# Kernel optimization log

Measured on AMD Instinct MI355X. Metric: run time of the kernel, lower is better.

The kernel has to match this reference:

```python
import jax, jax.numpy as jnp
import numpy as np

N_NODES = 100000


def gcn_conv(x, edge_index, W, b, num_nodes):
    # PyG GCNConv: h = x @ W; add self-loops; symmetric deg^-1/2 normalization;
    # out[dst] = sum_{src->dst} norm * h[src] + b
    h = x @ W
    loop = jnp.arange(num_nodes)
    src = jnp.concatenate([edge_index[0], loop])
    dst = jnp.concatenate([edge_index[1], loop])
    deg = jax.ops.segment_sum(jnp.ones_like(dst, dtype=h.dtype), dst, num_segments=num_nodes)
    dinv = jnp.where(deg > 0, jax.lax.rsqrt(deg), 0.0)
    norm = dinv[src] * dinv[dst]  # [E+N]
    msg = h[src] * norm[:, None]  # gather + scale
    out = jax.ops.segment_sum(msg, dst, num_segments=num_nodes)
    return out + b


def setup_inputs() -> dict:
    key = jax.random.key(0)
    k1, k2, k3, k4 = jax.random.split(key, 4)
    E = 3200000
    F_IN, HID, CLS = 512, 16, 7
    x = jax.random.normal(k1, (N_NODES, F_IN), dtype=jnp.float32)
    edge_index = jax.random.randint(k2, (2, E), 0, N_NODES, dtype=jnp.int64)
    W1 = jax.random.normal(k3, (F_IN, HID), dtype=jnp.float32) / np.sqrt(F_IN)
    b1 = jnp.zeros((HID,), dtype=jnp.float32)
    W2 = jax.random.normal(k4, (HID, CLS), dtype=jnp.float32) / np.sqrt(HID)
    b2 = jnp.zeros((CLS,), dtype=jnp.float32)
    return {"x": x, "edge_index": edge_index, "W1": W1, "b1": b1, "W2": W2, "b2": b2}


def reference(x, edge_index, W1, b1, W2, b2):
    h = gcn_conv(x, edge_index, W1, b1, N_NODES)
    h = jax.nn.relu(h)
    # dropout is identity in eval mode (p=0.5, training=False)
    out = gcn_conv(h, edge_index, W2, b2, N_NODES)
    return out
```

## Files before the change

### kernel.cpp

```cpp
#include <hip/hip_runtime.h>

#define N_NODES 100000
#define F_IN 512
#define HID 16
#define CLS 7

#define BK_SHIFT 8
#define BK_NODES 256
#define NBK ((N_NODES + BK_NODES - 1) / BK_NODES)
#define BK_CAP 9216

#define ADD4(a, v) { (a).x += (v).x; (a).y += (v).y; (a).z += (v).z; (a).w += (v).w; }
#define FMA4(acc, sc, wv) { (acc).x += (sc)*(wv).x; (acc).y += (sc)*(wv).y; (acc).z += (sc)*(wv).z; (acc).w += (sc)*(wv).w; }

__global__ void detect_i64_kernel(const unsigned int* __restrict__ idx32,
                                  int* __restrict__ flag, int n_check,
                                  int* __restrict__ cursor) {
    for (int i = threadIdx.x; i < NBK; i += blockDim.x) cursor[i] = 0;
    __shared__ unsigned int s;
    if (threadIdx.x == 0) s = 0u;
    __syncthreads();
    unsigned int v = 0u;
    for (int i = threadIdx.x; i < n_check; i += blockDim.x)
        v |= idx32[2 * i + 1];
    atomicOr(&s, v);
    __syncthreads();
    if (threadIdx.x == 0) *flag = (s == 0u) ? 1 : 0;
}

#define SB_T 512
#define SB_TILE 8192
#define SB_EPT (SB_TILE / SB_T)

__global__ __launch_bounds__(SB_T) void scatter_bin_kernel(const void* __restrict__ eidx,
                                                           long long E,
                                                           const int* __restrict__ flag,
                                                           int* __restrict__ cursor,
                                                           unsigned int* __restrict__ binned) {
    __shared__ int hist[NBK];
    __shared__ int gcur[NBK];
    const int is64 = *flag;
    const int tid = threadIdx.x;
    const long long tileBeg = (long long)blockIdx.x * SB_TILE;
    const bool evE = ((E & 1LL) == 0LL);

    for (int i = tid; i < NBK; i += SB_T) hist[i] = 0;
    __syncthreads();

    unsigned int vv[SB_EPT];
    int bb[SB_EPT];

#pragma unroll
    for (int j = 0; j < SB_EPT / 2; j++) {
        long long e = tileBeg + (long long)j * (2 * SB_T) + 2 * tid;
        int s0 = 0, d0 = 0, s1 = 0, d1 = 0;
        const bool ok0 = e < E, ok1 = (e + 1) < E;
        if (is64) {
            const long long* p = (const long long*)eidx;
            if (ok1 && evE) {
                longlong2 sp = *(const longlong2*)(p + e);
                longlong2 dp = *(const longlong2*)(p + E + e);
                s0 = (int)sp.x; s1 = (int)sp.y; d0 = (int)dp.x; d1 = (int)dp.y;
            } else {
                if (ok0) { s0 = (int)p[e];     d0 = (int)p[E + e]; }
                if (ok1) { s1 = (int)p[e + 1]; d1 = (int)p[E + e + 1]; }
            }
        } else {
            const int* p = (const int*)eidx;
            if (ok1 && evE) {
                int2 sp = *(const int2*)(p + e);
                int2 dp = *(const int2*)(p + E + e);
                s0 = sp.x; s1 = sp.y; d0 = dp.x; d1 = dp.y;
            } else {
                if (ok0) { s0 = p[e];     d0 = p[E + e]; }
                if (ok1) { s1 = p[e + 1]; d1 = p[E + e + 1]; }
            }
        }
        if (ok0) {
            int b = d0 >> BK_SHIFT;
            bb[2 * j] = b;
            vv[2 * j] = ((unsigned int)(d0 & (BK_NODES - 1)) << 17) | (unsigned int)s0;
            atomicAdd(&hist[b], 1);
        } else bb[2 * j] = -1;
        if (ok1) {
            int b = d1 >> BK_SHIFT;
            bb[2 * j + 1] = b;
            vv[2 * j + 1] = ((unsigned int)(d1 & (BK_NODES - 1)) << 17) | (unsigned int)s1;
            atomicAdd(&hist[b], 1);
        } else bb[2 * j + 1] = -1;
    }
    __syncthreads();
    for (int i = tid; i < NBK; i += SB_T)
        gcur[i] = hist[i] ? (i * BK_CAP + atomicAdd(&cursor[i], hist[i])) : 0;
    __syncthreads();
#pragma unroll
    for (int j = 0; j < SB_EPT; j++) {
        int b = bb[j];
        if (b >= 0) {
            int pos = atomicAdd(&gcur[b], 1);
            if (pos < (b + 1) * BK_CAP)
                binned[pos] = vv[j];
        }
    }
}

__global__ __launch_bounds__(512) void csr_build_kernel(const int* __restrict__ cursor,
                                                        unsigned int* __restrict__ binned,
                                                        float* __restrict__ dinv,
                                                        int* __restrict__ rowptr,
                                                        int* __restrict__ degA) {
    __shared__ unsigned int stage[BK_CAP];
    __shared__ int hist[BK_NODES];
    __shared__ int scanv[BK_NODES];
    __shared__ int curs[BK_NODES];
    const int tid = threadIdx.x;
    const int b = blockIdx.x;
    const int base = b * BK_CAP;
    int cnt = cursor[b];
    if (cnt > BK_CAP) cnt = BK_CAP;
    if (tid < BK_NODES) hist[tid] = 0;
    __syncthreads();
    const int cnt4 = cnt >> 2;
    for (int i = tid; i < cnt4; i += 512) {
        uint4 u = ((const uint4*)(binned + base))[i];
        ((uint4*)stage)[i] = u;
        atomicAdd(&hist[u.x >> 17], 1);
        atomicAdd(&hist[u.y >> 17], 1);
        atomicAdd(&hist[u.z >> 17], 1);
        atomicAdd(&hist[u.w >> 17], 1);
    }
    for (int i = (cnt4 << 2) + tid; i < cnt; i += 512) {
        unsigned int u = binned[base + i];
        stage[i] = u;
        atomicAdd(&hist[u >> 17], 1);
    }
    __syncthreads();
    if (tid < BK_NODES) scanv[tid] = hist[tid];
    __syncthreads();
    for (int off = 1; off < BK_NODES; off <<= 1) {
        int a = 0;
        if (tid < BK_NODES && tid >= off) a = scanv[tid - off];
        __syncthreads();
        if (tid < BK_NODES) scanv[tid] += a;
        __syncthreads();
    }
    if (tid < BK_NODES) {
        int e = scanv[tid] - hist[tid];
        curs[tid] = e;
        int g = b * BK_NODES + tid;
        if (g < N_NODES) {
            rowptr[g] = base + e;
            degA[g] = hist[tid];
            dinv[g] = rsqrtf((float)(hist[tid] + 1));
        }
    }
    __syncthreads();
    for (int i = tid; i < cnt4; i += 512) {
        uint4 u = ((const uint4*)stage)[i];
        int p0 = atomicAdd(&curs[(int)(u.x >> 17)], 1); binned[base + p0] = u.x & 0x1FFFFu;
        int p1 = atomicAdd(&curs[(int)(u.y >> 17)], 1); binned[base + p1] = u.y & 0x1FFFFu;
        int p2 = atomicAdd(&curs[(int)(u.z >> 17)], 1); binned[base + p2] = u.z & 0x1FFFFu;
        int p3 = atomicAdd(&curs[(int)(u.w >> 17)], 1); binned[base + p3] = u.w & 0x1FFFFu;
    }
    for (int i = (cnt4 << 2) + tid; i < cnt; i += 512) {
        unsigned int u = stage[i];
        int p = atomicAdd(&curs[(int)(u >> 17)], 1);
        binned[base + p] = u & 0x1FFFFu;
    }
}

#define G1_ROWS 128
#define G1_KC 32
#define G1_LDX (G1_KC + 4)

__global__ __launch_bounds__(256) void gemm1_kernel(const float* __restrict__ x,
                                                    const float* __restrict__ W1,
                                                    const float* __restrict__ dinv,
                                                    float* __restrict__ h1s) {
    __shared__ float Ws[F_IN * HID];
    __shared__ float xs[G1_ROWS][G1_LDX];
    const int tid = threadIdx.x;
    const int rowBase = blockIdx.x * G1_ROWS;

#pragma unroll
    for (int it = 0; it < 8; it++) {
        int f = it * 256 + tid;
        ((float4*)Ws)[f] = ((const float4*)W1)[f];
    }

    const int r  = tid >> 2;
    const int j4 = tid & 3;
    float4 accA = make_float4(0.f, 0.f, 0.f, 0.f);
    float4 accB = make_float4(0.f, 0.f, 0.f, 0.f);
    const float4* Wf4 = (const float4*)Ws;

    for (int kc = 0; kc < F_IN; kc += G1_KC) {
        __syncthreads();
#pragma unroll
        for (int it = 0; it < 4; it++) {
            int f = it * 256 + tid;
            int row = f >> 3;
            int c4 = f & 7;
            int grow = rowBase + row;
            if (grow >= N_NODES) grow = N_NODES - 1;
            *((float4*)&xs[row][c4 * 4]) = ((const float4*)(x + (long long)grow * F_IN + kc))[c4];
        }
        __syncthreads();
#pragma unroll
        for (int k4 = 0; k4 < G1_KC / 4; k4++) {
            float4 xa = *(const float4*)&xs[r][k4 * 4];
            float4 xb = *(const float4*)&xs[r + 64][k4 * 4];
            int kb = (kc + k4 * 4) * 4 + j4;
            float4 w0 = Wf4[kb];
            float4 w1 = Wf4[kb + 4];
            float4 w2 = Wf4[kb + 8];
            float4 w3 = Wf4[kb + 12];
            FMA4(accA, xa.x, w0); FMA4(accA, xa.y, w1);
            FMA4(accA, xa.z, w2); FMA4(accA, xa.w, w3);
            FMA4(accB, xb.x, w0); FMA4(accB, xb.y, w1);
            FMA4(accB, xb.z, w2); FMA4(accB, xb.w, w3);
        }
    }
    int g0 = rowBase + r;
    if (g0 < N_NODES) {
        float dn = dinv[g0];
        ((float4*)(h1s + (long long)g0 * HID))[j4] =
            make_float4(accA.x * dn, accA.y * dn, accA.z * dn, accA.w * dn);
    }
    int g1 = rowBase + 64 + r;
    if (g1 < N_NODES) {
        float dn = dinv[g1];
        ((float4*)(h1s + (long long)g1 * HID))[j4] =
            make_float4(accB.x * dn, accB.y * dn, accB.z * dn, accB.w * dn);
    }
}

#define A1_NODES 64

__global__ __launch_bounds__(256) void agg1_gemm2_kernel(const int* __restrict__ rowptr,
                                                         const int* __restrict__ degA,
                                                         const int* __restrict__ csr_src,
                                                         const float* __restrict__ h1s,
                                                         const float* __restrict__ dinv,
                                                         const float* __restrict__ b1,
                                                         const float* __restrict__ W2,
                                                         float* __restrict__ h2s) {
    __shared__ float W2s[HID][8];
    __shared__ float t_lds[A1_NODES][HID + 1];
    const int tid = threadIdx.x;
    if (tid < HID * 8) {
        int j = tid >> 3, c = tid & 7;
        W2s[j][c] = (c < CLS) ? W2[j * CLS + c] : 0.f;
    }
    const int ln = tid >> 2;
    const int j4 = tid & 3;
    const int n = blockIdx.x * A1_NODES + ln;
    float dn = 0.f;
    if (n < N_NODES) {
        const int beg = rowptr[n];
        const int end = beg + degA[n];
        const float4* h4 = (const float4*)h1s;
        float4 a0 = make_float4(0.f, 0.f, 0.f, 0.f);
        float4 a1 = make_float4(0.f, 0.f, 0.f, 0.f);
        float4 a2 = make_float4(0.f, 0.f, 0.f, 0.f);
        float4 a3 = make_float4(0.f, 0.f, 0.f, 0.f);
        int k = beg;
        for (; k < end && (k & 3); k++) {
            float4 v = h4[(long long)csr_src[k] * 4 + j4];
            ADD4(a0, v);
        }
        for (; k + 8 <= end; k += 8) {
            int4 s0 = *(const int4*)(csr_src + k);
            int4 s1 = *(const int4*)(csr_src + k + 4);
            float4 v0 = h4[(long long)s0.x * 4 + j4];
            float4 v1 = h4[(long long)s0.y * 4 + j4];
            float4 v2 = h4[(long long)s0.z * 4 + j4];
            float4 v3 = h4[(long long)s0.w * 4 + j4];
            float4 v4 = h4[(long long)s1.x * 4 + j4];
            float4 v5 = h4[(long long)s1.y * 4 + j4];
            float4 v6 = h4[(long long)s1.z * 4 + j4];
            float4 v7 = h4[(long long)s1.w * 4 + j4];
            ADD4(a0, v0); ADD4(a1, v1); ADD4(a2, v2); ADD4(a3, v3);
            ADD4(a0, v4); ADD4(a1, v5); ADD4(a2, v6); ADD4(a3, v7);
        }
        if (k + 4 <= end) {
            int4 s0 = *(const int4*)(csr_src + k);
            float4 v0 = h4[(long long)s0.x * 4 + j4];
            float4 v1 = h4[(long long)s0.y * 4 + j4];
            float4 v2 = h4[(long long)s0.z * 4 + j4];
            float4 v3 = h4[(long long)s0.w * 4 + j4];
            ADD4(a0, v0); ADD4(a1, v1); ADD4(a2, v2); ADD4(a3, v3);
            k += 4;
        }
        for (; k < end; k++) {
            float4 v = h4[(long long)csr_src[k] * 4 + j4];
            ADD4(a0, v);
        }
        dn = dinv[n];
        float4 self = h4[(long long)n * 4 + j4];
        float4 bb = ((const float4*)b1)[j4];
        float* tp = &t_lds[ln][j4 * 4];
        tp[0] = fmaxf(bb.x + dn * (a0.x + a1.x + a2.x + a3.x + self.x), 0.f);
        tp[1] = fmaxf(bb.y + dn * (a0.y + a1.y + a2.y + a3.y + self.y), 0.f);
        tp[2] = fmaxf(bb.z + dn * (a0.z + a1.z + a2.z + a3.z + self.z), 0.f);
        tp[3] = fmaxf(bb.w + dn * (a0.w + a1.w + a2.w + a3.w + self.w), 0.f);
    }
    __syncthreads();
    if (n < N_NODES) {
        float b0 = 0.f, c1 = 0.f;
#pragma unroll
        for (int j = 0; j < HID; j++) {
            float v = t_lds[ln][j];
            b0 += v * W2s[j][2 * j4];
            c1 += v * W2s[j][2 * j4 + 1];
        }
        h2s[(long long)n * 8 + 2 * j4]     = dn * b0;
        h2s[(long long)n * 8 + 2 * j4 + 1] = dn * c1;
    }
}

#define A2_NODES 128

__global__ __launch_bounds__(256) void agg2_gather_kernel(const int* __restrict__ rowptr,
                                                          const int* __restrict__ degA,
                                                          const int* __restrict__ csr_src,
                                                          const float* __restrict__ h2s,
                                                          const float* __restrict__ dinv,
                                                          const float* __restrict__ b2,
                                                          float* __restrict__ out) {
    const int tid = threadIdx.x;
    const int ln = tid >> 1;
    const int half = tid & 1;
    const int n = blockIdx.x * A2_NODES + ln;
    if (n >= N_NODES) return;
    const int beg = rowptr[n];
    const int end = beg + degA[n];
    const float4* h4 = (const float4*)h2s;
    float4 a0 = make_float4(0.f, 0.f, 0.f, 0.f);
    float4 a1 = make_float4(0.f, 0.f, 0.f, 0.f);
    float4 a2 = make_float4(0.f, 0.f, 0.f, 0.f);
    float4 a3 = make_float4(0.f, 0.f, 0.f, 0.f);
    int k = beg;
    for (; k < end && (k & 3); k++) {
        float4 v = h4[(long long)csr_src[k] * 2 + half];
        ADD4(a0, v);
    }
    for (; k + 8 <= end; k += 8) {
        int4 s0 = *(const int4*)(csr_src + k);
        int4 s1 = *(const int4*)(csr_src + k + 4);
        float4 v0 = h4[(long long)s0.x * 2 + half];
        float4 v1 = h4[(long long)s0.y * 2 + half];
        float4 v2 = h4[(long long)s0.z * 2 + half];
        float4 v3 = h4[(long long)s0.w * 2 + half];
        float4 v4 = h4[(long long)s1.x * 2 + half];
        float4 v5 = h4[(long long)s1.y * 2 + half];
        float4 v6 = h4[(long long)s1.z * 2 + half];
        float4 v7 = h4[(long long)s1.w * 2 + half];
        ADD4(a0, v0); ADD4(a1, v1); ADD4(a2, v2); ADD4(a3, v3);
        ADD4(a0, v4); ADD4(a1, v5); ADD4(a2, v6); ADD4(a3, v7);
    }
    if (k + 4 <= end) {
        int4 s0 = *(const int4*)(csr_src + k);
        float4 v0 = h4[(long long)s0.x * 2 + half];
        float4 v1 = h4[(long long)s0.y * 2 + half];
        float4 v2 = h4[(long long)s0.z * 2 + half];
        float4 v3 = h4[(long long)s0.w * 2 + half];
        ADD4(a0, v0); ADD4(a1, v1); ADD4(a2, v2); ADD4(a3, v3);
        k += 4;
    }
    for (; k < end; k++) {
        float4 v = h4[(long long)csr_src[k] * 2 + half];
        ADD4(a0, v);
    }
    float dn = dinv[n];
    float4 self = h4[(long long)n * 2 + half];
    float tx = self.x + a0.x + a1.x + a2.x + a3.x;
    float ty = self.y + a0.y + a1.y + a2.y + a3.y;
    float tz = self.z + a0.z + a1.z + a2.z + a3.z;
    float tw = self.w + a0.w + a1.w + a2.w + a3.w;
    long long ob = (long long)n * CLS;
    if (half == 0) {
        out[ob + 0] = b2[0] + dn * tx;
        out[ob + 1] = b2[1] + dn * ty;
        out[ob + 2] = b2[2] + dn * tz;
        out[ob + 3] = b2[3] + dn * tw;
    } else {
        out[ob + 4] = b2[4] + dn * tx;
        out[ob + 5] = b2[5] + dn * ty;
        out[ob + 6] = b2[6] + dn * tz;
    }
}

extern "C" void kernel_launch(void* const* d_in, const int* in_sizes, int n_in,
                              void* d_out, int out_size, void* d_ws, size_t ws_size,
                              hipStream_t stream) {
    const float* x    = (const float*)d_in[0];
    const void*  eidx = d_in[1];
    const float* W1   = (const float*)d_in[2];
    const float* b1   = (const float*)d_in[3];
    const float* W2   = (const float*)d_in[4];
    const float* b2   = (const float*)d_in[5];
    float* out = (float*)d_out;
    const long long E = (long long)in_sizes[1] / 2;

    char* ws = (char*)d_ws;
    size_t off = 0;
    auto alloc = [&](size_t bytes) -> void* {
        void* p = ws + off;
        off = (off + bytes + 255) & ~(size_t)255;
        return p;
    };
    int*          flag   = (int*)alloc(4);
    int*          cursor = (int*)alloc((size_t)NBK * 4);
    unsigned int* binned = (unsigned int*)alloc((size_t)NBK * BK_CAP * 4);
    int*          rowptr = (int*)alloc((size_t)N_NODES * 4);
    int*          degA   = (int*)alloc((size_t)N_NODES * 4);
    float*        dinv   = (float*)alloc((size_t)N_NODES * 4);
    float*        h1s    = (float*)alloc((size_t)N_NODES * HID * 4);
    float*        h2s    = (float*)alloc((size_t)N_NODES * 8 * 4);
    (void)ws_size;

    detect_i64_kernel<<<1, 256, 0, stream>>>((const unsigned int*)eidx, flag,
                                             (int)(E < 4096 ? E : 4096), cursor);

    scatter_bin_kernel<<<(int)((E + SB_TILE - 1) / SB_TILE), SB_T, 0, stream>>>(
        eidx, E, flag, cursor, binned);

    csr_build_kernel<<<NBK, 512, 0, stream>>>(cursor, binned, dinv, rowptr, degA);

    gemm1_kernel<<<(N_NODES + G1_ROWS - 1) / G1_ROWS, 256, 0, stream>>>(x, W1, dinv, h1s);

    const int* csr_src = (const int*)binned;
    agg1_gemm2_kernel<<<(N_NODES + A1_NODES - 1) / A1_NODES, 256, 0, stream>>>(
        rowptr, degA, csr_src, h1s, dinv, b1, W2, h2s);

    agg2_gather_kernel<<<(N_NODES + A2_NODES - 1) / A2_NODES, 256, 0, stream>>>(
        rowptr, degA, csr_src, h2s, dinv, b2, out);
}
```

Baseline: 450.3 us.

## Fuse edge binning and first GEMM into one kernel, defer dinv scaling

Merges the scatter-binning kernel and the x@W1 GEMM into a single launch, with blocks split by index so the memory-bound binning and the GEMM run concurrently on the GPU. This removes the serial dependency where the GEMM waited for degrees, so dinv scaling of h1 is moved into the CSR build kernel as a read-modify-write pass. The separate int64-detection kernel is replaced by a per-block check inside the fused kernel and a memset for the cursor reset. The cost is larger shared memory per block, which lowers occupancy, plus an extra global read and write of h1s.

```diff
diff --git a/kernel.cpp b/kernel.cpp
--- a/kernel.cpp
+++ b/kernel.cpp
@@ -10,97 +10,154 @@
 #define NBK ((N_NODES + BK_NODES - 1) / BK_NODES)
 #define BK_CAP 9216
 
+#define SB_TILE 4096
+#define SB_EPT 16
+
+#define G1_ROWS 128
+#define G1_KC 32
+#define G1_LDX (G1_KC + 4)
+
 #define ADD4(a, v) { (a).x += (v).x; (a).y += (v).y; (a).z += (v).z; (a).w += (v).w; }
 #define FMA4(acc, sc, wv) { (acc).x += (sc)*(wv).x; (acc).y += (sc)*(wv).y; (acc).z += (sc)*(wv).z; (acc).w += (sc)*(wv).w; }
 
-__global__ void detect_i64_kernel(const unsigned int* __restrict__ idx32,
-                                  int* __restrict__ flag, int n_check,
-                                  int* __restrict__ cursor) {
-    for (int i = threadIdx.x; i < NBK; i += blockDim.x) cursor[i] = 0;
-    __shared__ unsigned int s;
-    if (threadIdx.x == 0) s = 0u;
-    __syncthreads();
-    unsigned int v = 0u;
-    for (int i = threadIdx.x; i < n_check; i += blockDim.x)
-        v |= idx32[2 * i + 1];
-    atomicOr(&s, v);
-    __syncthreads();
-    if (threadIdx.x == 0) *flag = (s == 0u) ? 1 : 0;
-}
-
-#define SB_T 512
-#define SB_TILE 8192
-#define SB_EPT (SB_TILE / SB_T)
-
-__global__ __launch_bounds__(SB_T) void scatter_bin_kernel(const void* __restrict__ eidx,
-                                                           long long E,
-                                                           const int* __restrict__ flag,
-                                                           int* __restrict__ cursor,
-                                                           unsigned int* __restrict__ binned) {
+__global__ __launch_bounds__(256) void fat_kernel(const void* __restrict__ eidx,
+                                                  long long E,
+                                                  int* __restrict__ cursor,
+                                                  unsigned int* __restrict__ binned,
+                                                  const float* __restrict__ x,
+                                                  const float* __restrict__ W1,
+                                                  float* __restrict__ h1s,
+                                                  int scBlocks) {
+    __shared__ float Ws[F_IN * HID];
+    __shared__ float xs[G1_ROWS][G1_LDX];
     __shared__ int hist[NBK];
     __shared__ int gcur[NBK];
-    const int is64 = *flag;
+    __shared__ unsigned int det;
     const int tid = threadIdx.x;
-    const long long tileBeg = (long long)blockIdx.x * SB_TILE;
-    const bool evE = ((E & 1LL) == 0LL);
-
-    for (int i = tid; i < NBK; i += SB_T) hist[i] = 0;
-    __syncthreads();
-
-    unsigned int vv[SB_EPT];
-    int bb[SB_EPT];
-
-#pragma unroll
-    for (int j = 0; j < SB_EPT / 2; j++) {
-        long long e = tileBeg + (long long)j * (2 * SB_T) + 2 * tid;
-        int s0 = 0, d0 = 0, s1 = 0, d1 = 0;
-        const bool ok0 = e < E, ok1 = (e + 1) < E;
-        if (is64) {
-            const long long* p = (const long long*)eidx;
-            if (ok1 && evE) {
-                longlong2 sp = *(const longlong2*)(p + e);
-                longlong2 dp = *(const longlong2*)(p + E + e);
-                s0 = (int)sp.x; s1 = (int)sp.y; d0 = (int)dp.x; d1 = (int)dp.y;
+
+    if ((int)blockIdx.x < scBlocks) {
+        const long long tileBeg = (long long)blockIdx.x * SB_TILE;
+        long long remll = E - tileBeg;
+        const int tcnt = (int)(remll < SB_TILE ? remll : SB_TILE);
+        const bool evE = ((E & 1LL) == 0LL);
+
+        for (int i = tid; i < NBK; i += 256) hist[i] = 0;
+        if (tid == 0) det = 0u;
+        __syncthreads();
+
+        {
+            unsigned int myor = 0u;
+            const unsigned long long* p64 = (const unsigned long long*)eidx;
+            for (int i = tid; i < tcnt; i += 256)
+                myor |= (unsigned int)(p64[tileBeg + i] >> 32);
+            if (myor) atomicOr(&det, 1u);
+        }
+        __syncthreads();
+        const int is64 = (det == 0u) ? 1 : 0;
+
+        unsigned int vv[SB_EPT];
+        int bb[SB_EPT];
+
+#pragma unroll
+        for (int j = 0; j < SB_EPT / 2; j++) {
+            long long e = tileBeg + (long long)j * 512 + 2 * tid;
+            int s0 = 0, d0 = 0, s1 = 0, d1 = 0;
+            const bool ok0 = e < E, ok1 = (e + 1) < E;
+            if (is64) {
+                const long long* p = (const long long*)eidx;
+                if (ok1 && evE) {
+                    longlong2 sp = *(const longlong2*)(p + e);
+                    longlong2 dp = *(const longlong2*)(p + E + e);
+                    s0 = (int)sp.x; s1 = (int)sp.y; d0 = (int)dp.x; d1 = (int)dp.y;
+                } else {
+                    if (ok0) { s0 = (int)p[e];     d0 = (int)p[E + e]; }
+                    if (ok1) { s1 = (int)p[e + 1]; d1 = (int)p[E + e + 1]; }
+                }
             } else {
-                if (ok0) { s0 = (int)p[e];     d0 = (int)p[E + e]; }
-                if (ok1) { s1 = (int)p[e + 1]; d1 = (int)p[E + e + 1]; }
+                const int* p = (const int*)eidx;
+                if (ok1 && evE) {
+                    int2 sp = *(const int2*)(p + e);
+                    int2 dp = *(const int2*)(p + E + e);
+                    s0 = sp.x; s1 = sp.y; d0 = dp.x; d1 = dp.y;
+                } else {
+                    if (ok0) { s0 = p[e];     d0 = p[E + e]; }
+                    if (ok1) { s1 = p[e + 1]; d1 = p[E + e + 1]; }
+                }
             }
-        } else {
-            const int* p = (const int*)eidx;
-            if (ok1 && evE) {
-                int2 sp = *(const int2*)(p + e);
-                int2 dp = *(const int2*)(p + E + e);
-                s0 = sp.x; s1 = sp.y; d0 = dp.x; d1 = dp.y;
-            } else {
-                if (ok0) { s0 = p[e];     d0 = p[E + e]; }
-                if (ok1) { s1 = p[e + 1]; d1 = p[E + e + 1]; }
+            if (ok0) {
+                int b = d0 >> BK_SHIFT;
+                bb[2 * j] = b;
+                vv[2 * j] = ((unsigned int)(d0 & (BK_NODES - 1)) << 17) | (unsigned int)s0;
+                atomicAdd(&hist[b], 1);
+            } else bb[2 * j] = -1;
+            if (ok1) {
+                int b = d1 >> BK_SHIFT;
+                bb[2 * j + 1] = b;
+                vv[2 * j + 1] = ((unsigned int)(d1 & (BK_NODES - 1)) << 17) | (unsigned int)s1;
+                atomicAdd(&hist[b], 1);
+            } else bb[2 * j + 1] = -1;
+        }
+        __syncthreads();
+        for (int i = tid; i < NBK; i += 256)
+            gcur[i] = hist[i] ? (i * BK_CAP + atomicAdd(&cursor[i], hist[i])) : 0;
+        __syncthreads();
+#pragma unroll
+        for (int j = 0; j < SB_EPT; j++) {
+            int b = bb[j];
+            if (b >= 0) {
+                int pos = atomicAdd(&gcur[b], 1);
+                if (pos < (b + 1) * BK_CAP)
+                    binned[pos] = vv[j];
             }
         }
-        if (ok0) {
-            int b = d0 >> BK_SHIFT;
-            bb[2 * j] = b;
-            vv[2 * j] = ((unsigned int)(d0 & (BK_NODES - 1)) << 17) | (unsigned int)s0;
-            atomicAdd(&hist[b], 1);
-        } else bb[2 * j] = -1;
-        if (ok1) {
-            int b = d1 >> BK_SHIFT;
-            bb[2 * j + 1] = b;
-            vv[2 * j + 1] = ((unsigned int)(d1 & (BK_NODES - 1)) << 17) | (unsigned int)s1;
-            atomicAdd(&hist[b], 1);
-        } else bb[2 * j + 1] = -1;
-    }
-    __syncthreads();
-    for (int i = tid; i < NBK; i += SB_T)
-        gcur[i] = hist[i] ? (i * BK_CAP + atomicAdd(&cursor[i], hist[i])) : 0;
-    __syncthreads();
-#pragma unroll
-    for (int j = 0; j < SB_EPT; j++) {
-        int b = bb[j];
-        if (b >= 0) {
-            int pos = atomicAdd(&gcur[b], 1);
-            if (pos < (b + 1) * BK_CAP)
-                binned[pos] = vv[j];
-        }
+    } else {
+        const int rowBase = ((int)blockIdx.x - scBlocks) * G1_ROWS;
+
+#pragma unroll
+        for (int it = 0; it < 8; it++) {
+            int f = it * 256 + tid;
+            ((float4*)Ws)[f] = ((const float4*)W1)[f];
+        }
+
+        const int r  = tid >> 2;
+        const int j4 = tid & 3;
+        float4 accA = make_float4(0.f, 0.f, 0.f, 0.f);
+        float4 accB = make_float4(0.f, 0.f, 0.f, 0.f);
+        const float4* Wf4 = (const float4*)Ws;
+
+        for (int kc = 0; kc < F_IN; kc += G1_KC) {
+            __syncthreads();
+#pragma unroll
+            for (int it = 0; it < 4; it++) {
+                int f = it * 256 + tid;
+                int row = f >> 3;
+                int c4 = f & 7;
+                int grow = rowBase + row;
+                if (grow >= N_NODES) grow = N_NODES - 1;
+                *((float4*)&xs[row][c4 * 4]) = ((const float4*)(x + (long long)grow * F_IN + kc))[c4];
+            }
+            __syncthreads();
+#pragma unroll
+            for (int k4 = 0; k4 < G1_KC / 4; k4++) {
+                float4 xa = *(const float4*)&xs[r][k4 * 4];
+                float4 xb = *(const float4*)&xs[r + 64][k4 * 4];
+                int kb = (kc + k4 * 4) * 4 + j4;
+                float4 w0 = Wf4[kb];
+                float4 w1 = Wf4[kb + 4];
+                float4 w2 = Wf4[kb + 8];
+                float4 w3 = Wf4[kb + 12];
+                FMA4(accA, xa.x, w0); FMA4(accA, xa.y, w1);
+                FMA4(accA, xa.z, w2); FMA4(accA, xa.w, w3);
+                FMA4(accB, xb.x, w0); FMA4(accB, xb.y, w1);
+                FMA4(accB, xb.z, w2); FMA4(accB, xb.w, w3);
+            }
+        }
+        int g0 = rowBase + r;
+        if (g0 < N_NODES)
+            ((float4*)(h1s + (long long)g0 * HID))[j4] = accA;
+        int g1 = rowBase + 64 + r;
+        if (g1 < N_NODES)
+            ((float4*)(h1s + (long long)g1 * HID))[j4] = accB;
     }
 }
 
@@ -108,7 +165,8 @@
                                                         unsigned int* __restrict__ binned,
                                                         float* __restrict__ dinv,
                                                         int* __restrict__ rowptr,
-                                                        int* __restrict__ degA) {
+                                                        int* __restrict__ degA,
+                                                        float* __restrict__ h1s) {
     __shared__ unsigned int stage[BK_CAP];
     __shared__ int hist[BK_NODES];
     __shared__ int scanv[BK_NODES];
@@ -167,71 +225,18 @@
         int p = atomicAdd(&curs[(int)(u >> 17)], 1);
         binned[base + p] = u & 0x1FFFFu;
     }
-}
-
-#define G1_ROWS 128
-#define G1_KC 32
-#define G1_LDX (G1_KC + 4)
-
-__global__ __launch_bounds__(256) void gemm1_kernel(const float* __restrict__ x,
-                                                    const float* __restrict__ W1,
-                                                    const float* __restrict__ dinv,
-                                                    float* __restrict__ h1s) {
-    __shared__ float Ws[F_IN * HID];
-    __shared__ float xs[G1_ROWS][G1_LDX];
-    const int tid = threadIdx.x;
-    const int rowBase = blockIdx.x * G1_ROWS;
-
-#pragma unroll
-    for (int it = 0; it < 8; it++) {
-        int f = it * 256 + tid;
-        ((float4*)Ws)[f] = ((const float4*)W1)[f];
-    }
-
-    const int r  = tid >> 2;
-    const int j4 = tid & 3;
-    float4 accA = make_float4(0.f, 0.f, 0.f, 0.f);
-    float4 accB = make_float4(0.f, 0.f, 0.f, 0.f);
-    const float4* Wf4 = (const float4*)Ws;
-
-    for (int kc = 0; kc < F_IN; kc += G1_KC) {
-        __syncthreads();
-#pragma unroll
-        for (int it = 0; it < 4; it++) {
-            int f = it * 256 + tid;
-            int row = f >> 3;
-            int c4 = f & 7;
-            int grow = rowBase + row;
-            if (grow >= N_NODES) grow = N_NODES - 1;
-            *((float4*)&xs[row][c4 * 4]) = ((const float4*)(x + (long long)grow * F_IN + kc))[c4];
-        }
-        __syncthreads();
-#pragma unroll
-        for (int k4 = 0; k4 < G1_KC / 4; k4++) {
-            float4 xa = *(const float4*)&xs[r][k4 * 4];
-            float4 xb = *(const float4*)&xs[r + 64][k4 * 4];
-            int kb = (kc + k4 * 4) * 4 + j4;
-            float4 w0 = Wf4[kb];
-            float4 w1 = Wf4[kb + 4];
-            float4 w2 = Wf4[kb + 8];
-            float4 w3 = Wf4[kb + 12];
-            FMA4(accA, xa.x, w0); FMA4(accA, xa.y, w1);
-            FMA4(accA, xa.z, w2); FMA4(accA, xa.w, w3);
-            FMA4(accB, xb.x, w0); FMA4(accB, xb.y, w1);
-            FMA4(accB, xb.z, w2); FMA4(accB, xb.w, w3);
-        }
-    }
-    int g0 = rowBase + r;
-    if (g0 < N_NODES) {
-        float dn = dinv[g0];
-        ((float4*)(h1s + (long long)g0 * HID))[j4] =
-            make_float4(accA.x * dn, accA.y * dn, accA.z * dn, accA.w * dn);
-    }
-    int g1 = rowBase + 64 + r;
-    if (g1 < N_NODES) {
-        float dn = dinv[g1];
-        ((float4*)(h1s + (long long)g1 * HID))[j4] =
-            make_float4(accB.x * dn, accB.y * dn, accB.z * dn, accB.w * dn);
+    {
+        const int ln = tid >> 1;
+        const int hf = tid & 1;
+        const int g = b * BK_NODES + ln;
+        if (g < N_NODES) {
+            float dn = rsqrtf((float)(hist[ln] + 1));
+            float4* hp = (float4*)(h1s + (long long)g * HID);
+            float4 v0 = hp[hf * 2];
+            float4 v1 = hp[hf * 2 + 1];
+            hp[hf * 2]     = make_float4(v0.x * dn, v0.y * dn, v0.z * dn, v0.w * dn);
+            hp[hf * 2 + 1] = make_float4(v1.x * dn, v1.y * dn, v1.z * dn, v1.w * dn);
+        }
     }
 }
 
@@ -410,7 +415,6 @@
         off = (off + bytes + 255) & ~(size_t)255;
         return p;
     };
-    int*          flag   = (int*)alloc(4);
     int*          cursor = (int*)alloc((size_t)NBK * 4);
     unsigned int* binned = (unsigned int*)alloc((size_t)NBK * BK_CAP * 4);
     int*          rowptr = (int*)alloc((size_t)N_NODES * 4);
@@ -420,15 +424,14 @@
     float*        h2s    = (float*)alloc((size_t)N_NODES * 8 * 4);
     (void)ws_size;
 
-    detect_i64_kernel<<<1, 256, 0, stream>>>((const unsigned int*)eidx, flag,
-                                             (int)(E < 4096 ? E : 4096), cursor);
-
-    scatter_bin_kernel<<<(int)((E + SB_TILE - 1) / SB_TILE), SB_T, 0, stream>>>(
-        eidx, E, flag, cursor, binned);
-
-    csr_build_kernel<<<NBK, 512, 0, stream>>>(cursor, binned, dinv, rowptr, degA);
-
-    gemm1_kernel<<<(N_NODES + G1_ROWS - 1) / G1_ROWS, 256, 0, stream>>>(x, W1, dinv, h1s);
+    hipMemsetAsync(cursor, 0, (size_t)NBK * 4, stream);
+
+    const int scBlocks = (int)((E + SB_TILE - 1) / SB_TILE);
+    const int gmBlocks = (N_NODES + G1_ROWS - 1) / G1_ROWS;
+    fat_kernel<<<scBlocks + gmBlocks, 256, 0, stream>>>(
+        eidx, E, cursor, binned, x, W1, h1s, scBlocks);
+
+    csr_build_kernel<<<NBK, 512, 0, stream>>>(cursor, binned, dinv, rowptr, degA, h1s);
 
     const int* csr_src = (const int*)binned;
     agg1_gemm2_kernel<<<(N_NODES + A1_NODES - 1) / A1_NODES, 256, 0, stream>>>(
```

Result: faster. 440.0 us (-2.3%).
